# Kernel tuning notes

Measured on AMD Instinct MI355X. Metric: run time of the kernel, lower is better.

## Reference

```python
import jax, jax.numpy as jnp
import numpy as np

H = 12  # n_heads

def setup_inputs() -> dict:
    key = jax.random.key(0)
    ks = jax.random.split(key, 7)
    dim = 768
    x = jax.random.normal(ks[0], (2, 8, 4, 256, dim), dtype=jnp.float32)
    s = dim ** -0.5
    Wq = jax.random.normal(ks[1], (dim, dim), dtype=jnp.float32) * s
    bq = jax.random.normal(ks[2], (dim,), dtype=jnp.float32) * 0.01
    Wk = jax.random.normal(ks[3], (dim, dim), dtype=jnp.float32) * s
    bk = jax.random.normal(ks[4], (dim,), dtype=jnp.float32) * 0.01
    Wv = jax.random.normal(ks[5], (dim, dim), dtype=jnp.float32) * s
    bv = jax.random.normal(ks[6], (dim,), dtype=jnp.float32) * 0.01
    return {"x": x, "Wq": Wq, "bq": bq, "Wk": Wk, "bk": bk, "Wv": Wv, "bv": bv}

def _split_heads(y):
    # [b,t,l,p,(h d)] -> [b,t,l,h,p,d]
    b, t, l, p, hd = y.shape
    return y.reshape(b, t, l, p, H, hd // H).transpose(0, 1, 2, 4, 3, 5)

def reference(x, Wq, bq, Wk, bk, Wv, bv):
    dim = x.shape[-1]
    scale = (dim / H) ** -0.5
    q = _split_heads(x @ Wq.T + bq)  # [b,t,l,h,p,d]
    k = _split_heads(x @ Wk.T + bk)
    v = _split_heads(x @ Wv.T + bv)
    dots = jnp.einsum('btlhpd,btlhqd->btlhpq', q, k) * scale
    attn = jax.nn.softmax(dots, axis=-1)
    out = jnp.einsum('btlhpq,btlhqd->btlhpd', attn, v)
    # [b,t,l,h,p,d] -> [b,t,l,p,(h d)]
    b, t, l, h, p, d = out.shape
    return out.transpose(0, 1, 2, 4, 3, 5).reshape(b, t, l, p, h * d)
```

## Files before the change

kernel.cpp:

```cpp
#include <hip/hip_runtime.h>

typedef _Float16 f16;
typedef __attribute__((ext_vector_type(2))) _Float16 f16x2;
typedef __attribute__((ext_vector_type(8))) _Float16 f16x8;
typedef __attribute__((ext_vector_type(4))) float f32x4;

#define MFMA16(a,b,c) __builtin_amdgcn_mfma_f32_16x16x32_f16(a,b,c,0,0,0)

constexpr int NSEQ = 64;
constexpr int P    = 256;
constexpr int DIMF = 768;
constexpr int NH   = 12;
constexpr int DH   = 64;
constexpr int M    = NSEQ * P;
constexpr size_t XSZ = (size_t)M * DIMF;
constexpr size_t WSZ = (size_t)DIMF * DIMF;

__device__ __forceinline__ f16x8 cvt8(const float* p) {
    const float4 u = *(const float4*)p;
    const float4 w = *(const float4*)(p + 4);
    f16x2 a = __builtin_bit_cast(f16x2, __builtin_amdgcn_cvt_pkrtz(u.x, u.y));
    f16x2 b = __builtin_bit_cast(f16x2, __builtin_amdgcn_cvt_pkrtz(u.z, u.w));
    f16x2 c = __builtin_bit_cast(f16x2, __builtin_amdgcn_cvt_pkrtz(w.x, w.y));
    f16x2 d = __builtin_bit_cast(f16x2, __builtin_amdgcn_cvt_pkrtz(w.z, w.w));
    f16x8 r;
    r[0]=a[0]; r[1]=a[1]; r[2]=b[0]; r[3]=b[1];
    r[4]=c[0]; r[5]=c[1]; r[6]=d[0]; r[7]=d[1];
    return r;
}

__device__ __forceinline__ void gload16(const void* g, void* l) {
    __builtin_amdgcn_global_load_lds(
        (const __attribute__((address_space(1))) void*)g,
        (__attribute__((address_space(3))) void*)l, 16, 0, 0);
}

__global__ __launch_bounds__(256) void conv_kernel(
    const float* __restrict__ x,
    const float* __restrict__ Wq, const float* __restrict__ Wk,
    const float* __restrict__ Wv,
    f16* __restrict__ xh, f16* __restrict__ wh)
{
    const size_t i8 = ((size_t)blockIdx.x * 256 + threadIdx.x) * 8;
    if (i8 < XSZ) {
        *(f16x8*)(xh + i8) = cvt8(x + i8);
    } else {
        const size_t j = i8 - XSZ;
        const int mtx = (int)(j / WSZ);
        const size_t r = j - (size_t)mtx * WSZ;
        const float* src = (mtx == 0 ? Wq : mtx == 1 ? Wk : Wv) + r;
        *(f16x8*)(wh + j) = cvt8(src);
    }
}

__global__ __launch_bounds__(512, 1) void proj_gemm(
    const f16* __restrict__ xh, const f16* __restrict__ wh,
    const float* __restrict__ bq, const float* __restrict__ bk,
    const float* __restrict__ bv,
    f16* __restrict__ qout, f16* __restrict__ kout, f16* __restrict__ vt)
{
    __shared__ __align__(16) char smem[131072];
    const int wg = (blockIdx.x & 7) * 72 + (blockIdx.x >> 3);
    const int nt = wg % 9;
    const int mt = wg / 9;
    const int m0 = mt * 256, n0 = nt * 256;

    const int tid  = threadIdx.x;
    const int lane = tid & 63;
    const int wave = tid >> 6;
    const int lr   = lane & 15;
    const int lg   = lane >> 4;
    const int wm   = wave >> 2;
    const int wn   = wave & 3;

    const f16* srcA = xh + (size_t)(m0 + (tid >> 3)) * DIMF + ((tid & 7) ^ ((tid >> 3) & 7)) * 8;
    const f16* srcB = wh + (size_t)(n0 + (tid >> 3)) * DIMF + ((tid & 7) ^ ((tid >> 3) & 7)) * 8;
    char* dA = smem + tid * 16;
    char* dB = smem + 65536 + tid * 16;

    const int swz0 = (lg ^ (lr & 7)) * 16;
    const char* rA = smem + (wm * 64 + lr) * 128;
    const char* rB = smem + 65536 + (wn * 32 + lr) * 128;

    f32x4 acc[2][4][2][2];
    #pragma unroll
    for (int ah = 0; ah < 2; ++ah)
      #pragma unroll
      for (int m = 0; m < 4; ++m)
        #pragma unroll
        for (int bh = 0; bh < 2; ++bh)
          #pragma unroll
          for (int n = 0; n < 2; ++n) acc[ah][m][bh][n] = (f32x4){0.f,0.f,0.f,0.f};

    f16x8 a[4][2], bf0[2][2], bf1[2][2];

    #define ST_A(H, T, B) do {                                                    \
        gload16(srcA + (size_t)((H)*128      ) * DIMF + (T)*64, dA + (B)*32768 + (H)*16384);          \
        gload16(srcA + (size_t)((H)*128 + 64 ) * DIMF + (T)*64, dA + (B)*32768 + (H)*16384 + 8192); } while (0)
    #define ST_B(H, T, B) do {                                                    \
        gload16(srcB + (size_t)((H)*128      ) * DIMF + (T)*64, dB + (B)*32768 + (H)*16384);          \
        gload16(srcB + (size_t)((H)*128 + 64 ) * DIMF + (T)*64, dB + (B)*32768 + (H)*16384 + 8192); } while (0)

    #define RD_A(H, B) do { _Pragma("unroll")                                      \
        for (int m = 0; m < 4; ++m) {                                              \
            a[m][0] = *(const f16x8*)(rA + (B)*32768 + (H)*16384 + m*2048 + swz0);        \
            a[m][1] = *(const f16x8*)(rA + (B)*32768 + (H)*16384 + m*2048 + (swz0^64)); } } while (0)
    #define RD_B(H, B, BF) do { _Pragma("unroll")                                  \
        for (int n = 0; n < 2; ++n) {                                              \
            BF[n][0] = *(const f16x8*)(rB + (B)*32768 + (H)*16384 + n*2048 + swz0);       \
            BF[n][1] = *(const f16x8*)(rB + (B)*32768 + (H)*16384 + n*2048 + (swz0^64)); } } while (0)

    #define CLUSTER(AH, BH, BF) do {                                               \
        __builtin_amdgcn_s_setprio(1);                                             \
        _Pragma("unroll") for (int m = 0; m < 4; ++m)                              \
        _Pragma("unroll") for (int n = 0; n < 2; ++n) {                            \
            acc[AH][m][BH][n] = MFMA16(a[m][0], BF[n][0], acc[AH][m][BH][n]);      \
            acc[AH][m][BH][n] = MFMA16(a[m][1], BF[n][1], acc[AH][m][BH][n]); }    \
        __builtin_amdgcn_s_setprio(0); } while (0)

    #define BAR  __builtin_amdgcn_s_barrier()
    #define LGKM asm volatile("s_waitcnt lgkmcnt(0)" ::: "memory")
    #define SCHB __builtin_amdgcn_sched_barrier(0)
    #define VM(N) asm volatile("s_waitcnt vmcnt(" #N ")" ::: "memory")

    ST_A(0, 0, 0); ST_B(0, 0, 0); ST_B(1, 0, 0); ST_A(1, 0, 0);
    VM(0);
    BAR;

    for (int it = 0; it < 6; ++it) {
        const int T = 2 * it;
        const bool st2 = it < 5;

        RD_A(0, 0); RD_B(0, 0, bf0);
        ST_A(0, T + 1, 1); ST_B(0, T + 1, 1);
        VM(6); BAR; LGKM; SCHB;
        CLUSTER(0, 0, bf0);

        RD_B(1, 0, bf1);
        ST_B(1, T + 1, 1);
        VM(6); BAR; LGKM; SCHB;
        CLUSTER(0, 1, bf1);

        RD_A(1, 0);
        ST_A(1, T + 1, 1);
        BAR; LGKM; SCHB;
        CLUSTER(1, 1, bf1);

        VM(4); BAR; SCHB;
        CLUSTER(1, 0, bf0);

        RD_A(0, 1); RD_B(0, 1, bf0);
        if (st2) { ST_A(0, T + 2, 0); ST_B(0, T + 2, 0); }
        if (st2) { VM(6); } else { VM(2); }
        BAR; LGKM; SCHB;
        CLUSTER(0, 0, bf0);

        RD_B(1, 1, bf1);
        if (st2) ST_B(1, T + 2, 0);
        if (st2) { VM(6); } else { VM(0); }
        BAR; LGKM; SCHB;
        CLUSTER(0, 1, bf1);

        RD_A(1, 1);
        if (st2) ST_A(1, T + 2, 0);
        BAR; LGKM; SCHB;
        CLUSTER(1, 1, bf1);

        VM(4); BAR; SCHB;
        CLUSTER(1, 0, bf0);
    }

    __syncthreads();

    const int mat = nt / 3;
    const int c0  = (nt % 3) * 256;
    const int seq = mt;
    const float* __restrict__ bias = mat == 0 ? bq : mat == 1 ? bk : bv;
    float bb[2][2];
    #pragma unroll
    for (int bh = 0; bh < 2; ++bh)
        #pragma unroll
        for (int n = 0; n < 2; ++n)
            bb[bh][n] = bias[c0 + bh*128 + wn*32 + n*16 + lr];

    f16 (*ep)[264] = (f16 (*)[264])smem;
    #pragma unroll
    for (int hh = 0; hh < 2; ++hh) {
        #pragma unroll
        for (int m = 0; m < 4; ++m)
            #pragma unroll
            for (int bh = 0; bh < 2; ++bh)
                #pragma unroll
                for (int n = 0; n < 2; ++n)
                    #pragma unroll
                    for (int i = 0; i < 4; ++i)
                        ep[wm*64 + m*16 + lg*4 + i][bh*128 + wn*32 + n*16 + lr] =
                            (f16)(acc[hh][m][bh][n][i] + bb[bh][n]);
        __syncthreads();
        if (mat < 2) {
            f16* __restrict__ dst = mat ? kout : qout;
            const int r = tid >> 2;
            #pragma unroll
            for (int s = 0; s < 8; ++s) {
                const int ch = s*4 + (tid & 3);
                const int h  = (nt % 3) * 4 + (ch >> 3);
                const int d0 = (ch & 7) * 8;
                *(f16x8*)(dst + ((size_t)(seq*NH + h)*P + hh*128 + r)*DH + d0) =
                    *(const f16x8*)&ep[r][ch*8];
            }
        } else {
            const int col = tid >> 1, rg = tid & 1;
            const int h = (nt % 3) * 4 + (col >> 6), d = col & 63;
            f16* drow = vt + ((size_t)(seq*NH + h)*DH + d)*P + hh*128 + rg*64;
            #pragma unroll
            for (int u = 0; u < 8; ++u) {
                f16x8 vv;
                #pragma unroll
                for (int uu = 0; uu < 8; ++uu)
                    vv[uu] = ep[rg*64 + u*8 + uu][col];
                *(f16x8*)(drow + u*8) = vv;
            }
        }
        __syncthreads();
    }
    #undef ST_A
    #undef ST_B
    #undef RD_A
    #undef RD_B
    #undef CLUSTER
    #undef BAR
    #undef LGKM
    #undef SCHB
    #undef VM
}

__global__ __launch_bounds__(512) void attn_kernel(
    const f16* __restrict__ q, const f16* __restrict__ k,
    const f16* __restrict__ vt, float* __restrict__ out)
{
    __shared__ __align__(16) char kl[32768];
    __shared__ __align__(16) char vl[32768];
    __shared__ __align__(16) char pl[8][2048];

    const int n = blockIdx.x;
    const int b = (n & 7) * 192 + (n >> 3);
    const int half = b & 1;
    const int head = (b >> 1) % NH;
    const int seq  = b / (2 * NH);

    const int tid  = threadIdx.x;
    const int lane = tid & 63;
    const int wave = tid >> 6;
    const int lr   = lane & 15;
    const int lg   = lane >> 4;

    const f16* qh = q  + (size_t)(seq*NH + head)*P*DH;
    const f16* kh = k  + (size_t)(seq*NH + head)*P*DH;
    const f16* vh = vt + (size_t)(seq*NH + head)*DH*P;

    {
        const int r0 = tid >> 3, ck = tid & 7;
        const int d0 = tid >> 5, cv = tid & 31;
        #pragma unroll
        for (int it = 0; it < 4; ++it) {
            const int row = it * 64 + r0;
            gload16(kh + row * 64 + ((ck ^ (row & 7)) * 8), kl + it * 8192 + tid * 16);
            const int d = it * 16 + d0;
            gload16(vh + d * 256 + (((cv & 24) | ((cv ^ d) & 7)) * 8), vl + it * 8192 + tid * 16);
        }
    }

    const int qr0 = half * 128 + wave * 16;
    const f16x8 aq0 = *(const f16x8*)(qh + (qr0 + lr) * DH + lg * 8);
    const f16x8 aq1 = *(const f16x8*)(qh + (qr0 + lr) * DH + 32 + lg * 8);

    __syncthreads();

    f32x4 s[16];
    #pragma unroll
    for (int t = 0; t < 16; ++t) s[t] = (f32x4){0.f,0.f,0.f,0.f};
    __builtin_amdgcn_s_setprio(1);
    #pragma unroll
    for (int t = 0; t < 16; ++t) {
        const int row = t * 16 + lr;
        const f16x8 b0 = *(const f16x8*)(kl + row * 128 + ((lg ^ (row & 7)) * 16));
        const f16x8 b1 = *(const f16x8*)(kl + row * 128 + (((lg + 4) ^ (row & 7)) * 16));
        s[t] = MFMA16(aq0, b0, s[t]);
        s[t] = MFMA16(aq1, b1, s[t]);
    }
    __builtin_amdgcn_s_setprio(0);

    float mx[4] = {-1e30f, -1e30f, -1e30f, -1e30f};
    #pragma unroll
    for (int t = 0; t < 16; ++t)
        #pragma unroll
        for (int i = 0; i < 4; ++i) mx[i] = fmaxf(mx[i], s[t][i]);
    #pragma unroll
    for (int st = 1; st < 16; st <<= 1)
        #pragma unroll
        for (int i = 0; i < 4; ++i) mx[i] = fmaxf(mx[i], __shfl_xor(mx[i], st));

    const float SCL = 0.125f * 1.44269504088896f;
    float rs[4] = {0.f, 0.f, 0.f, 0.f};
    #pragma unroll
    for (int t = 0; t < 16; ++t)
        #pragma unroll
        for (int i = 0; i < 4; ++i) {
            const float e = exp2f((s[t][i] - mx[i]) * SCL);
            s[t][i] = e;
            rs[i] += e;
        }
    #pragma unroll
    for (int st = 1; st < 16; st <<= 1)
        #pragma unroll
        for (int i = 0; i < 4; ++i) rs[i] += __shfl_xor(rs[i], st);

    char* pw = pl[wave];
    f32x4 o[4];
    #pragma unroll
    for (int t = 0; t < 4; ++t) o[t] = (f32x4){0.f,0.f,0.f,0.f};

    #pragma unroll
    for (int qq = 0; qq < 4; ++qq) {
        #pragma unroll
        for (int tt = 0; tt < 4; ++tt) {
            const int t = qq * 4 + tt;
            #pragma unroll
            for (int i = 0; i < 4; ++i) {
                const int r = lg * 4 + i;
                const int klocal = tt * 16 + lr;
                *(f16*)(pw + r * 128 + ((klocal * 2) ^ ((r & 7) << 4))) = (f16)s[t][i];
            }
        }
        __builtin_amdgcn_s_setprio(1);
        #pragma unroll
        for (int kol = 0; kol < 2; ++kol) {
            const f16x8 ap = *(const f16x8*)(pw + lr * 128 + (((kol * 4 + lg) ^ (lr & 7)) * 16));
            #pragma unroll
            for (int dt = 0; dt < 4; ++dt) {
                const int row = dt * 16 + lr;
                const int ch  = qq * 8 + kol * 4 + lg;
                const f16x8 bv_ = *(const f16x8*)(vl + row * 512 + (((ch & 24) | ((ch ^ row) & 7)) * 16));
                o[dt] = MFMA16(ap, bv_, o[dt]);
            }
        }
        __builtin_amdgcn_s_setprio(0);
    }

    #pragma unroll
    for (int i = 0; i < 4; ++i) rs[i] = 1.f / rs[i];
    float* op = out + ((size_t)seq * P + qr0) * DIMF + head * DH;
    #pragma unroll
    for (int t = 0; t < 4; ++t)
        #pragma unroll
        for (int i = 0; i < 4; ++i)
            op[(lg * 4 + i) * DIMF + t * 16 + lr] = o[t][i] * rs[i];
}

extern "C" void kernel_launch(void* const* d_in, const int* in_sizes, int n_in,
                              void* d_out, int out_size, void* d_ws, size_t ws_size,
                              hipStream_t stream) {
    const float* x  = (const float*)d_in[0];
    const float* Wq = (const float*)d_in[1];
    const float* bq = (const float*)d_in[2];
    const float* Wk = (const float*)d_in[3];
    const float* bk = (const float*)d_in[4];
    const float* Wv = (const float*)d_in[5];
    const float* bv = (const float*)d_in[6];
    float* out = (float*)d_out;

    f16* xh = (f16*)d_out;
    f16* wh = xh + XSZ;

    const size_t QSZ = (size_t)M * DIMF;
    f16* q  = (f16*)d_ws;
    f16* k  = q + QSZ;
    f16* vt = k + QSZ;

    const int convThreads = (int)((XSZ + 3 * WSZ) / 8);
    conv_kernel<<<convThreads / 256, 256, 0, stream>>>(x, Wq, Wk, Wv, xh, wh);
    proj_gemm<<<dim3(576), 512, 0, stream>>>(xh, wh, bq, bk, bv, q, k, vt);
    attn_kernel<<<dim3(NSEQ * NH * 2), 512, 0, stream>>>(q, k, vt, out);
}
```

Baseline: 119.8 us.

## Switch projection GEMM to 256x192 tiles with simpler double-buffered pipeline

Changes the QKV projection GEMM tile from 256x256 to 256x192, raising the grid from 576 to 768 workgroups. With 256 CUs this gives exactly three waves instead of a partial third wave. The old 8-stage interleaved schedule with per-half B fragments becomes a simpler two-buffer TILE macro that loads a full K-tile, then runs two MFMA clusters while the next tile streams in. The epilogue is adjusted for three heads per tile and idle threads in the V transpose. In exchange, each tile has lower arithmetic intensity and the schedule overlaps loads and compute less finely.

```diff
diff --git a/kernel.cpp b/kernel.cpp
--- a/kernel.cpp
+++ b/kernel.cpp
@@ -59,11 +59,11 @@
     const float* __restrict__ bv,
     f16* __restrict__ qout, f16* __restrict__ kout, f16* __restrict__ vt)
 {
-    __shared__ __align__(16) char smem[131072];
-    const int wg = (blockIdx.x & 7) * 72 + (blockIdx.x >> 3);
-    const int nt = wg % 9;
-    const int mt = wg / 9;
-    const int m0 = mt * 256, n0 = nt * 256;
+    __shared__ __align__(16) char smem[114688];
+    const int wg = (blockIdx.x & 7) * 96 + (blockIdx.x >> 3);
+    const int nt = wg % 12;
+    const int mt = wg / 12;
+    const int m0 = mt * 256, n0 = nt * 192;
 
     const int tid  = threadIdx.x;
     const int lane = tid & 63;
@@ -80,158 +80,129 @@
 
     const int swz0 = (lg ^ (lr & 7)) * 16;
     const char* rA = smem + (wm * 64 + lr) * 128;
-    const char* rB = smem + 65536 + (wn * 32 + lr) * 128;
-
-    f32x4 acc[2][4][2][2];
+    const char* rB = smem + 65536 + (wn * 48 + lr) * 128;
+
+    f32x4 acc[2][4][3];
     #pragma unroll
     for (int ah = 0; ah < 2; ++ah)
       #pragma unroll
       for (int m = 0; m < 4; ++m)
         #pragma unroll
-        for (int bh = 0; bh < 2; ++bh)
-          #pragma unroll
-          for (int n = 0; n < 2; ++n) acc[ah][m][bh][n] = (f32x4){0.f,0.f,0.f,0.f};
-
-    f16x8 a[4][2], bf0[2][2], bf1[2][2];
-
-    #define ST_A(H, T, B) do {                                                    \
-        gload16(srcA + (size_t)((H)*128      ) * DIMF + (T)*64, dA + (B)*32768 + (H)*16384);          \
+        for (int n = 0; n < 3; ++n) acc[ah][m][n] = (f32x4){0.f,0.f,0.f,0.f};
+
+    f16x8 a[4][2], bf[3][2];
+
+    #define STA(H, T, B) do {                                                     \
+        gload16(srcA + (size_t)((H)*128      ) * DIMF + (T)*64, dA + (B)*32768 + (H)*16384);         \
         gload16(srcA + (size_t)((H)*128 + 64 ) * DIMF + (T)*64, dA + (B)*32768 + (H)*16384 + 8192); } while (0)
-    #define ST_B(H, T, B) do {                                                    \
-        gload16(srcB + (size_t)((H)*128      ) * DIMF + (T)*64, dB + (B)*32768 + (H)*16384);          \
-        gload16(srcB + (size_t)((H)*128 + 64 ) * DIMF + (T)*64, dB + (B)*32768 + (H)*16384 + 8192); } while (0)
-
-    #define RD_A(H, B) do { _Pragma("unroll")                                      \
-        for (int m = 0; m < 4; ++m) {                                              \
-            a[m][0] = *(const f16x8*)(rA + (B)*32768 + (H)*16384 + m*2048 + swz0);        \
+    #define STB(U, T, B)                                                          \
+        gload16(srcB + (size_t)((U)*64) * DIMF + (T)*64, dB + (B)*24576 + (U)*8192)
+
+    #define RD_A(H, B) do { _Pragma("unroll")                                     \
+        for (int m = 0; m < 4; ++m) {                                             \
+            a[m][0] = *(const f16x8*)(rA + (B)*32768 + (H)*16384 + m*2048 + swz0);       \
             a[m][1] = *(const f16x8*)(rA + (B)*32768 + (H)*16384 + m*2048 + (swz0^64)); } } while (0)
-    #define RD_B(H, B, BF) do { _Pragma("unroll")                                  \
-        for (int n = 0; n < 2; ++n) {                                              \
-            BF[n][0] = *(const f16x8*)(rB + (B)*32768 + (H)*16384 + n*2048 + swz0);       \
-            BF[n][1] = *(const f16x8*)(rB + (B)*32768 + (H)*16384 + n*2048 + (swz0^64)); } } while (0)
-
-    #define CLUSTER(AH, BH, BF) do {                                               \
-        __builtin_amdgcn_s_setprio(1);                                             \
-        _Pragma("unroll") for (int m = 0; m < 4; ++m)                              \
-        _Pragma("unroll") for (int n = 0; n < 2; ++n) {                            \
-            acc[AH][m][BH][n] = MFMA16(a[m][0], BF[n][0], acc[AH][m][BH][n]);      \
-            acc[AH][m][BH][n] = MFMA16(a[m][1], BF[n][1], acc[AH][m][BH][n]); }    \
+    #define RD_BALL(B) do { _Pragma("unroll")                                     \
+        for (int n = 0; n < 3; ++n) {                                             \
+            bf[n][0] = *(const f16x8*)(rB + (B)*24576 + n*2048 + swz0);           \
+            bf[n][1] = *(const f16x8*)(rB + (B)*24576 + n*2048 + (swz0^64)); } } while (0)
+
+    #define CLUSTER(AH) do {                                                      \
+        __builtin_amdgcn_s_setprio(1);                                            \
+        _Pragma("unroll") for (int m = 0; m < 4; ++m)                             \
+        _Pragma("unroll") for (int n = 0; n < 3; ++n) {                           \
+            acc[AH][m][n] = MFMA16(a[m][0], bf[n][0], acc[AH][m][n]);             \
+            acc[AH][m][n] = MFMA16(a[m][1], bf[n][1], acc[AH][m][n]); }           \
         __builtin_amdgcn_s_setprio(0); } while (0)
 
     #define BAR  __builtin_amdgcn_s_barrier()
     #define LGKM asm volatile("s_waitcnt lgkmcnt(0)" ::: "memory")
     #define SCHB __builtin_amdgcn_sched_barrier(0)
-    #define VM(N) asm volatile("s_waitcnt vmcnt(" #N ")" ::: "memory")
-
-    ST_A(0, 0, 0); ST_B(0, 0, 0); ST_B(1, 0, 0); ST_A(1, 0, 0);
-    VM(0);
-    BAR;
+
+    #define TILE(T, B, ST) do {                                                   \
+        BAR;                  \
+        if (ST) { STA(0, (T)+1, (B)^1); STB(0, (T)+1, (B)^1); STB(1, (T)+1, (B)^1);  \
+                  SCHB; asm volatile("s_waitcnt vmcnt(4)" ::: "memory"); }        \
+        else    { asm volatile("s_waitcnt vmcnt(0)" ::: "memory"); }              \
+        BAR;                                                  \
+        SCHB;                                                                     \
+        RD_A(0, B); RD_BALL(B);                                                   \
+        LGKM; SCHB;                                                               \
+        CLUSTER(0);                                                               \
+        if (ST) { STA(1, (T)+1, (B)^1); STB(2, (T)+1, (B)^1); }                   \
+        RD_A(1, B);                                                               \
+        LGKM; SCHB;                                                               \
+        CLUSTER(1);                                                               \
+    } while (0)
+
+    STA(0, 0, 0); STB(0, 0, 0); STB(1, 0, 0);
+    STA(1, 0, 0); STB(2, 0, 0);
 
     for (int it = 0; it < 6; ++it) {
-        const int T = 2 * it;
-        const bool st2 = it < 5;
-
-        RD_A(0, 0); RD_B(0, 0, bf0);
-        ST_A(0, T + 1, 1); ST_B(0, T + 1, 1);
-        VM(6); BAR; LGKM; SCHB;
-        CLUSTER(0, 0, bf0);
-
-        RD_B(1, 0, bf1);
-        ST_B(1, T + 1, 1);
-        VM(6); BAR; LGKM; SCHB;
-        CLUSTER(0, 1, bf1);
-
-        RD_A(1, 0);
-        ST_A(1, T + 1, 1);
-        BAR; LGKM; SCHB;
-        CLUSTER(1, 1, bf1);
-
-        VM(4); BAR; SCHB;
-        CLUSTER(1, 0, bf0);
-
-        RD_A(0, 1); RD_B(0, 1, bf0);
-        if (st2) { ST_A(0, T + 2, 0); ST_B(0, T + 2, 0); }
-        if (st2) { VM(6); } else { VM(2); }
-        BAR; LGKM; SCHB;
-        CLUSTER(0, 0, bf0);
-
-        RD_B(1, 1, bf1);
-        if (st2) ST_B(1, T + 2, 0);
-        if (st2) { VM(6); } else { VM(0); }
-        BAR; LGKM; SCHB;
-        CLUSTER(0, 1, bf1);
-
-        RD_A(1, 1);
-        if (st2) ST_A(1, T + 2, 0);
-        BAR; LGKM; SCHB;
-        CLUSTER(1, 1, bf1);
-
-        VM(4); BAR; SCHB;
-        CLUSTER(1, 0, bf0);
+        TILE(2*it,     0, true);
+        TILE(2*it + 1, 1, (it < 5));
     }
 
     __syncthreads();
 
-    const int mat = nt / 3;
-    const int c0  = (nt % 3) * 256;
+    const int mat = nt >> 2;
+    const int c0  = (nt & 3) * 192;
+    const int h0  = (nt & 3) * 3;
     const int seq = mt;
     const float* __restrict__ bias = mat == 0 ? bq : mat == 1 ? bk : bv;
-    float bb[2][2];
-    #pragma unroll
-    for (int bh = 0; bh < 2; ++bh)
-        #pragma unroll
-        for (int n = 0; n < 2; ++n)
-            bb[bh][n] = bias[c0 + bh*128 + wn*32 + n*16 + lr];
-
-    f16 (*ep)[264] = (f16 (*)[264])smem;
+    float bb[3];
+    #pragma unroll
+    for (int n = 0; n < 3; ++n) bb[n] = bias[c0 + wn*48 + n*16 + lr];
+
+    f16 (*ep)[200] = (f16 (*)[200])smem;
     #pragma unroll
     for (int hh = 0; hh < 2; ++hh) {
         #pragma unroll
         for (int m = 0; m < 4; ++m)
             #pragma unroll
-            for (int bh = 0; bh < 2; ++bh)
+            for (int n = 0; n < 3; ++n)
                 #pragma unroll
-                for (int n = 0; n < 2; ++n)
-                    #pragma unroll
-                    for (int i = 0; i < 4; ++i)
-                        ep[wm*64 + m*16 + lg*4 + i][bh*128 + wn*32 + n*16 + lr] =
-                            (f16)(acc[hh][m][bh][n][i] + bb[bh][n]);
+                for (int i = 0; i < 4; ++i)
+                    ep[wm*64 + m*16 + lg*4 + i][wn*48 + n*16 + lr] =
+                        (f16)(acc[hh][m][n][i] + bb[n]);
         __syncthreads();
         if (mat < 2) {
             f16* __restrict__ dst = mat ? kout : qout;
             const int r = tid >> 2;
             #pragma unroll
-            for (int s = 0; s < 8; ++s) {
+            for (int s = 0; s < 6; ++s) {
                 const int ch = s*4 + (tid & 3);
-                const int h  = (nt % 3) * 4 + (ch >> 3);
+                const int h  = h0 + (ch >> 3);
                 const int d0 = (ch & 7) * 8;
                 *(f16x8*)(dst + ((size_t)(seq*NH + h)*P + hh*128 + r)*DH + d0) =
                     *(const f16x8*)&ep[r][ch*8];
             }
         } else {
-            const int col = tid >> 1, rg = tid & 1;
-            const int h = (nt % 3) * 4 + (col >> 6), d = col & 63;
-            f16* drow = vt + ((size_t)(seq*NH + h)*DH + d)*P + hh*128 + rg*64;
-            #pragma unroll
-            for (int u = 0; u < 8; ++u) {
-                f16x8 vv;
+            if (tid < 384) {
+                const int col = tid >> 1, rg = tid & 1;
+                const int h = h0 + (col >> 6), d = col & 63;
+                f16* drow = vt + ((size_t)(seq*NH + h)*DH + d)*P + hh*128 + rg*64;
                 #pragma unroll
-                for (int uu = 0; uu < 8; ++uu)
-                    vv[uu] = ep[rg*64 + u*8 + uu][col];
-                *(f16x8*)(drow + u*8) = vv;
+                for (int u = 0; u < 8; ++u) {
+                    f16x8 vv;
+                    #pragma unroll
+                    for (int uu = 0; uu < 8; ++uu)
+                        vv[uu] = ep[rg*64 + u*8 + uu][col];
+                    *(f16x8*)(drow + u*8) = vv;
+                }
             }
         }
         __syncthreads();
     }
-    #undef ST_A
-    #undef ST_B
+    #undef STA
+    #undef STB
     #undef RD_A
-    #undef RD_B
+    #undef RD_BALL
     #undef CLUSTER
     #undef BAR
     #undef LGKM
     #undef SCHB
-    #undef VM
+    #undef TILE
 }
 
 __global__ __launch_bounds__(512) void attn_kernel(
@@ -379,6 +350,6 @@
 
     const int convThreads = (int)((XSZ + 3 * WSZ) / 8);
     conv_kernel<<<convThreads / 256, 256, 0, stream>>>(x, Wq, Wk, Wv, xh, wh);
-    proj_gemm<<<dim3(576), 512, 0, stream>>>(xh, wh, bq, bk, bv, q, k, vt);
+    proj_gemm<<<dim3(768), 512, 0, stream>>>(xh, wh, bq, bk, bv, q, k, vt);
     attn_kernel<<<dim3(NSEQ * NH * 2), 512, 0, stream>>>(q, k, vt, out);
 }
```

Result: faster. 115.9 us (-3.3%).
